# Performance work log

Hardware: AMD Instinct MI355X
Metric: run time of the kernel (lower is better)

Reference implementation:

```python
import jax, jax.numpy as jnp
import numpy as np

B, S, D, H = 2, 1536, 1024, 16
DK = D // H
NEG = -1e9
WEIGHT = 1.0  # undefined global `Weight` in source; treated as scalar 1.0


def setup_inputs() -> dict:
    key = jax.random.key(0)
    ks = jax.random.split(key, 16)
    inp = {
        "query": jax.random.normal(ks[0], (B, S, D), jnp.float32),
        "key": jax.random.normal(ks[1], (B, S, D), jnp.float32),
        "value": jax.random.normal(ks[2], (B, S, D), jnp.float32),
        "mask": jax.random.randint(ks[3], (B, 1, 1, S), 0, 2, jnp.int32),
        "mask1": jax.random.randint(ks[4], (B, 1, S, S), 0, 2, jnp.int32).astype(jnp.float32),
        "Wq": jax.random.normal(ks[5], (D, D), jnp.float32) / np.sqrt(D),
        "bq": jnp.zeros((D,), jnp.float32),
        "Wk": jax.random.normal(ks[6], (D, D), jnp.float32) / np.sqrt(D),
        "bk": jnp.zeros((D,), jnp.float32),
        "Wv": jax.random.normal(ks[7], (D, D), jnp.float32) / np.sqrt(D),
        "bv": jnp.zeros((D,), jnp.float32),
        "Wo": jax.random.normal(ks[8], (D, D), jnp.float32) / np.sqrt(D),
        "bo": jnp.zeros((D,), jnp.float32),
    }
    return inp


def _split_heads(x):
    # [B,S,D] -> [B,H,S,DK]
    return x.reshape(B, S, H, DK).transpose(0, 2, 1, 3)


def reference(query, key, value, mask, mask1, Wq, bq, Wk, bk, Wv, bv, Wo, bo):
    q = _split_heads(query @ Wq.T + bq)
    k = _split_heads(key @ Wk.T + bk)
    v = _split_heads(value @ Wv.T + bv)

    scores = jnp.einsum("bhqd,bhkd->bhqk", q, k) / jnp.sqrt(jnp.float32(DK))
    # softmax of mask1 over the query axis (dim=-2), zeros masked out
    m1 = jnp.where(mask1 == 0, NEG, mask1)
    m1s = jax.nn.softmax(m1, axis=-2)
    scores = (1.0 + m1s * mask1) * scores * WEIGHT
    scores = jnp.where(mask == 0, NEG, scores)
    p = jax.nn.softmax(scores, axis=-1)  # dropout: eval mode (identity)
    x = jnp.einsum("bhqk,bhkd->bhqd", p, v)
    x = x.transpose(0, 2, 1, 3).reshape(B, S, D)
    ret = x @ Wo.T + bo
    return ret, scores
```

## Files before the change

kernel.cpp:

```cpp
#include <hip/hip_runtime.h>
#include <hip/hip_bf16.h>

#define B_ 2
#define S_ 1536
#define D_ 1024
#define H_ 16
#define DK_ 64
#define KW_ 48
#define NT_ 24

#define RET_ELEMS 3145728

typedef __attribute__((ext_vector_type(8))) short short8;
typedef __attribute__((ext_vector_type(8))) unsigned short ushort8v;
typedef __attribute__((ext_vector_type(4))) unsigned short ushort4v;
typedef __attribute__((ext_vector_type(4))) float f32x4;

__device__ __forceinline__ unsigned short bf16_rne(float f) {
    return __builtin_bit_cast(unsigned short, __float2bfloat16(f));
}

struct CvtJobs {
    const float* src[7];
    unsigned short* dst[7];
    int n8[7];
};

__global__ __launch_bounds__(256) void cvt_kernel(CvtJobs j) {
    const int y = blockIdx.y;
    const int i = blockIdx.x * 256 + threadIdx.x;
    if (i >= j.n8[y]) return;
    const float* s = j.src[y] + (size_t)i * 8;
    float4 f0 = *(const float4*)s;
    float4 f1 = *(const float4*)(s + 4);
    ushort8v u;
    u[0]=bf16_rne(f0.x); u[1]=bf16_rne(f0.y); u[2]=bf16_rne(f0.z); u[3]=bf16_rne(f0.w);
    u[4]=bf16_rne(f1.x); u[5]=bf16_rne(f1.y); u[6]=bf16_rne(f1.z); u[7]=bf16_rne(f1.w);
    *(ushort8v*)(j.dst[y] + (size_t)i * 8) = u;
}

__global__ void bitpack_kernel(const float* __restrict__ mask1, unsigned int* __restrict__ bits,
                               float* __restrict__ colsum) {
    if (blockIdx.x < 12) colsum[blockIdx.x * 256 + threadIdx.x] = 0.f;
    const size_t gid = (size_t)blockIdx.x * 256 + threadIdx.x;
    const float v = mask1[gid];
    const unsigned long long bal = __ballot(v != 0.f);
    const int l = threadIdx.x & 63;
    if (l == 0)       bits[gid >> 5] = (unsigned int)bal;
    else if (l == 32) bits[gid >> 5] = (unsigned int)(bal >> 32);
}

__global__ void colcount_bits_kernel(const unsigned int* __restrict__ bits, float* __restrict__ colsum) {
    const int b     = blockIdx.x / 6;
    const int chunk = blockIdx.x % 6;
    const int col   = chunk * 256 + threadIdx.x;
    const int q0    = blockIdx.y * 96;
    const int wword = col >> 5, bit = col & 31;
    const unsigned int* p = bits + ((size_t)b * S_ + q0) * KW_ + wword;
    int s = 0;
    #pragma unroll 8
    for (int q = 0; q < 96; ++q) s += (p[(size_t)q * KW_] >> bit) & 1u;
    atomicAdd(&colsum[b * S_ + col], (float)s);
}

struct Proj { const unsigned short* A; const unsigned short* W; const float* bias; unsigned short* C; };

__global__ __launch_bounds__(512) void qkv_gemm_kernel(Proj p0, Proj p1, Proj p2) {
    const int bid = blockIdx.x;
    const int xcd = bid & 7, idx = bid >> 3;
    const int zy = xcd * 9 + (idx >> 3);
    const int bx = idx & 7;
    const int z = zy / 24, by = zy % 24;

    const unsigned short* A = z == 0 ? p0.A    : (z == 1 ? p1.A    : p2.A);
    const unsigned short* W = z == 0 ? p0.W    : (z == 1 ? p1.W    : p2.W);
    const float* bias       = z == 0 ? p0.bias : (z == 1 ? p1.bias : p2.bias);
    unsigned short* C       = z == 0 ? p0.C    : (z == 1 ? p1.C    : p2.C);

    __shared__ unsigned short As[128][72];
    __shared__ unsigned short Bs[128][72];
    const int tid = threadIdx.x;
    const int w = tid >> 6, lane = tid & 63;
    const int g = lane >> 4, c = lane & 15;
    const int wm = w >> 2, wn = w & 3;
    const int m0 = by * 128, n0 = bx * 128;
    const int trow = tid >> 2;
    const int tcol = (tid & 3) * 16;

    f32x4 acc[4][2];
    #pragma unroll
    for (int m = 0; m < 4; ++m)
        #pragma unroll
        for (int n = 0; n < 2; ++n)
            acc[m][n] = f32x4{0.f, 0.f, 0.f, 0.f};

    for (int k0 = 0; k0 < D_; k0 += 64) {
        {
            const unsigned short* ap = A + (size_t)(m0 + trow) * D_ + k0 + tcol;
            *(ushort8v*)&As[trow][tcol]     = *(const ushort8v*)ap;
            *(ushort8v*)&As[trow][tcol + 8] = *(const ushort8v*)(ap + 8);
            const unsigned short* wp = W + (size_t)(n0 + trow) * D_ + k0 + tcol;
            *(ushort8v*)&Bs[trow][tcol]     = *(const ushort8v*)wp;
            *(ushort8v*)&Bs[trow][tcol + 8] = *(const ushort8v*)(wp + 8);
        }
        __syncthreads();
        #pragma unroll
        for (int kk = 0; kk < 2; ++kk) {
            short8 a[4], bb[2];
            #pragma unroll
            for (int m = 0; m < 4; ++m) a[m]  = *(const short8*)&As[wm * 64 + m * 16 + c][kk * 32 + g * 8];
            #pragma unroll
            for (int n = 0; n < 2; ++n) bb[n] = *(const short8*)&Bs[wn * 32 + n * 16 + c][kk * 32 + g * 8];
            __builtin_amdgcn_s_setprio(1);
            #pragma unroll
            for (int m = 0; m < 4; ++m)
                #pragma unroll
                for (int n = 0; n < 2; ++n)
                    acc[m][n] = __builtin_amdgcn_mfma_f32_16x16x32_bf16(a[m], bb[n], acc[m][n], 0, 0, 0);
            __builtin_amdgcn_s_setprio(0);
        }
        __syncthreads();
    }
    #pragma unroll
    for (int n = 0; n < 2; ++n) {
        const int col = n0 + wn * 32 + n * 16 + c;
        const float bval = bias[col];
        #pragma unroll
        for (int m = 0; m < 4; ++m) {
            const int row0 = m0 + wm * 64 + m * 16 + g * 4;
            #pragma unroll
            for (int r = 0; r < 4; ++r)
                C[(size_t)(row0 + r) * D_ + col] = bf16_rne(acc[m][n][r] + bval);
        }
    }
}

__global__ __launch_bounds__(256) void out_gemm_kernel(
    const unsigned short* __restrict__ A, const unsigned short* __restrict__ W,
    const float* __restrict__ bias, float* __restrict__ C)
{
    const int bid = blockIdx.x;
    const int xcd = bid & 7, idx = bid >> 3;
    const int yg = xcd * 6 + (idx >> 4);
    const int bx = idx & 15;

    __shared__ unsigned short As[64][72];
    __shared__ unsigned short Bs[64][72];
    const int tid = threadIdx.x;
    const int w = tid >> 6, lane = tid & 63;
    const int g = lane >> 4, c = lane & 15;
    const int wm = w >> 1, wn = w & 1;
    const int m0 = yg * 64, n0 = bx * 64;
    const int trow = tid >> 2;
    const int tcol = (tid & 3) * 16;

    f32x4 acc[2][2];
    #pragma unroll
    for (int m = 0; m < 2; ++m)
        #pragma unroll
        for (int n = 0; n < 2; ++n)
            acc[m][n] = f32x4{0.f, 0.f, 0.f, 0.f};

    for (int k0 = 0; k0 < D_; k0 += 64) {
        {
            const unsigned short* ap = A + (size_t)(m0 + trow) * D_ + k0 + tcol;
            *(ushort8v*)&As[trow][tcol]     = *(const ushort8v*)ap;
            *(ushort8v*)&As[trow][tcol + 8] = *(const ushort8v*)(ap + 8);
            const unsigned short* wp = W + (size_t)(n0 + trow) * D_ + k0 + tcol;
            *(ushort8v*)&Bs[trow][tcol]     = *(const ushort8v*)wp;
            *(ushort8v*)&Bs[trow][tcol + 8] = *(const ushort8v*)(wp + 8);
        }
        __syncthreads();
        #pragma unroll
        for (int kk = 0; kk < 2; ++kk) {
            short8 a[2], bb[2];
            #pragma unroll
            for (int m = 0; m < 2; ++m) a[m]  = *(const short8*)&As[wm * 32 + m * 16 + c][kk * 32 + g * 8];
            #pragma unroll
            for (int n = 0; n < 2; ++n) bb[n] = *(const short8*)&Bs[wn * 32 + n * 16 + c][kk * 32 + g * 8];
            __builtin_amdgcn_s_setprio(1);
            #pragma unroll
            for (int m = 0; m < 2; ++m)
                #pragma unroll
                for (int n = 0; n < 2; ++n)
                    acc[m][n] = __builtin_amdgcn_mfma_f32_16x16x32_bf16(a[m], bb[n], acc[m][n], 0, 0, 0);
            __builtin_amdgcn_s_setprio(0);
        }
        __syncthreads();
    }
    #pragma unroll
    for (int n = 0; n < 2; ++n) {
        const int col = n0 + wn * 32 + n * 16 + c;
        const float bval = bias[col];
        #pragma unroll
        for (int m = 0; m < 2; ++m) {
            const int row0 = m0 + wm * 32 + m * 16 + g * 4;
            #pragma unroll
            for (int r = 0; r < 4; ++r)
                C[(size_t)(row0 + r) * D_ + col] = acc[m][n][r] + bval;
        }
    }
}

__global__ __launch_bounds__(512) void attn_kernel(
    const unsigned short* __restrict__ Qb, const unsigned short* __restrict__ Kb,
    const unsigned short* __restrict__ Vb, const int* __restrict__ mask,
    const unsigned int* __restrict__ bits, const float* __restrict__ colsum,
    float* __restrict__ scores, unsigned short* __restrict__ X)
{
    const int bid = blockIdx.x;
    const int xcd = bid & 7, idx = bid >> 3;
    const int grp = xcd * 4 + idx / 12;
    const int qt  = idx % 12;
    const int h = grp & 15, b = grp >> 4;

    const int tid = threadIdx.x;
    const int w = tid >> 6, lane = tid & 63;
    const int g = lane >> 4, c = lane & 15;

    __shared__ unsigned short VT_lds[2][64][72];
    __shared__ unsigned short P_lds[8][16][72];
    __shared__ float fac_lds[S_];

    for (int i = tid; i < S_; i += 512) {
        const int km = mask[b * S_ + i];
        const float cnt = colsum[b * S_ + i];
        fac_lds[i] = (km == 0) ? -1.f : ((cnt > 0.f) ? (1.f / cnt) : 0.f);
    }

    const int qrow0 = qt * 128 + w * 16;
    const unsigned short* qptr = Qb + ((size_t)b * S_ + qrow0 + c) * D_ + h * DK_;
    const short8 qf0 = *(const short8*)(qptr + g * 8);
    const short8 qf1 = *(const short8*)(qptr + 32 + g * 8);

    float mrow = -INFINITY, lrow = 0.f;
    f32x4 o[4];
    #pragma unroll
    for (int n = 0; n < 4; ++n) o[n] = f32x4{0.f, 0.f, 0.f, 0.f};

    float* srow = scores + ((((size_t)(b * H_ + h)) * S_ + qrow0 + c) * S_);
    const unsigned int* brow = bits + ((size_t)b * S_ + qrow0 + c) * KW_;
    const int kr = tid & 63, half = tid >> 6;
    const unsigned short* vrow = Vb + ((size_t)b * S_ + kr) * D_ + h * DK_ + half * 8;

    {
        short8 v0 = *(const short8*)vrow;
        #pragma unroll
        for (int j = 0; j < 8; ++j)
            VT_lds[0][half * 8 + j][kr] = (unsigned short)v0[j];
    }
    __syncthreads();

    for (int kt = 0; kt < NT_; ++kt) {
        const int k0 = kt * 64;
        const int cur = kt & 1;
        const bool have_next = (kt + 1) < NT_;

        short8 nv0;
        if (have_next) nv0 = *(const short8*)(vrow + (size_t)(k0 + 64) * D_);

        f32x4 sacc[4];
        #pragma unroll
        for (int n = 0; n < 4; ++n) sacc[n] = f32x4{0.f, 0.f, 0.f, 0.f};
        short8 kf0[4], kf1[4];
        #pragma unroll
        for (int n = 0; n < 4; ++n) {
            const unsigned short* kp = Kb + ((size_t)b * S_ + k0 + n * 16 + c) * D_ + h * DK_;
            kf0[n] = *(const short8*)(kp + g * 8);
            kf1[n] = *(const short8*)(kp + 32 + g * 8);
        }
        __builtin_amdgcn_s_setprio(1);
        #pragma unroll
        for (int n = 0; n < 4; ++n) {
            sacc[n] = __builtin_amdgcn_mfma_f32_16x16x32_bf16(kf0[n], qf0, sacc[n], 0, 0, 0);
            sacc[n] = __builtin_amdgcn_mfma_f32_16x16x32_bf16(kf1[n], qf1, sacc[n], 0, 0, 0);
        }
        __builtin_amdgcn_s_setprio(0);

        const unsigned int w0 = brow[(k0 >> 5)];
        const unsigned int w1 = brow[(k0 >> 5) + 1];
        float pmax = -INFINITY;
        f32x4 sv[4];
        #pragma unroll
        for (int n = 0; n < 4; ++n) {
            const f32x4 fv = *(const f32x4*)&fac_lds[k0 + n * 16 + g * 4];
            const unsigned int wsel = (n < 2) ? w0 : w1;
            #pragma unroll
            for (int r = 0; r < 4; ++r) {
                const int kl = n * 16 + g * 4 + r;
                const float f = fv[r];
                const float icnt = fmaxf(f, 0.f);
                const float bit = (float)((wsel >> (kl & 31)) & 1u);
                float s = sacc[n][r] * 0.125f * (1.f + bit * icnt);
                s = (f < 0.f) ? -1e9f : s;
                sv[n][r] = s;
                pmax = fmaxf(pmax, s);
            }
            __builtin_nontemporal_store(sv[n], (f32x4*)&srow[k0 + n * 16 + g * 4]);
        }

        pmax = fmaxf(pmax, __shfl_xor(pmax, 16));
        pmax = fmaxf(pmax, __shfl_xor(pmax, 32));
        const float nm = fmaxf(mrow, pmax);
        const float scq = __expf(mrow - nm);
        mrow = nm;
        lrow *= scq;
        float sc_o[4];
        #pragma unroll
        for (int r = 0; r < 4; ++r) sc_o[r] = __shfl(scq, (lane & 48) | (g * 4 + r));
        #pragma unroll
        for (int n = 0; n < 4; ++n)
            #pragma unroll
            for (int r = 0; r < 4; ++r) o[n][r] *= sc_o[r];

        #pragma unroll
        for (int n = 0; n < 4; ++n) {
            ushort4v pu;
            #pragma unroll
            for (int r = 0; r < 4; ++r) {
                const float p = __expf(sv[n][r] - mrow);
                lrow += p;
                pu[r] = bf16_rne(p);
            }
            *(ushort4v*)&P_lds[w][c][n * 16 + g * 4] = pu;
        }

        if (have_next) {
            #pragma unroll
            for (int j = 0; j < 8; ++j)
                VT_lds[cur ^ 1][half * 8 + j][kr] = (unsigned short)nv0[j];
        }

        __builtin_amdgcn_s_setprio(1);
        #pragma unroll
        for (int kk = 0; kk < 2; ++kk) {
            const short8 pa = *(const short8*)&P_lds[w][c][kk * 32 + g * 8];
            #pragma unroll
            for (int n = 0; n < 4; ++n) {
                const short8 vf = *(const short8*)&VT_lds[cur][n * 16 + c][kk * 32 + g * 8];
                o[n] = __builtin_amdgcn_mfma_f32_16x16x32_bf16(pa, vf, o[n], 0, 0, 0);
            }
        }
        __builtin_amdgcn_s_setprio(0);
        __syncthreads();
    }

    lrow += __shfl_xor(lrow, 16);
    lrow += __shfl_xor(lrow, 32);
    const float linv = 1.f / lrow;
    float linv_o[4];
    #pragma unroll
    for (int r = 0; r < 4; ++r) linv_o[r] = __shfl(linv, (lane & 48) | (g * 4 + r));
    #pragma unroll
    for (int n = 0; n < 4; ++n)
        #pragma unroll
        for (int r = 0; r < 4; ++r) {
            const size_t idx = ((size_t)b * S_ + qrow0 + g * 4 + r) * D_ + h * DK_ + n * 16 + c;
            X[idx] = bf16_rne(o[n][r] * linv_o[r]);
        }
}

extern "C" void kernel_launch(void* const* d_in, const int* in_sizes, int n_in,
                              void* d_out, int out_size, void* d_ws, size_t ws_size,
                              hipStream_t stream) {
    const float* query = (const float*)d_in[0];
    const float* key   = (const float*)d_in[1];
    const float* value = (const float*)d_in[2];
    const int*   mask  = (const int*)d_in[3];
    const float* mask1 = (const float*)d_in[4];
    const float* Wq = (const float*)d_in[5];
    const float* bq = (const float*)d_in[6];
    const float* Wk = (const float*)d_in[7];
    const float* bk = (const float*)d_in[8];
    const float* Wv = (const float*)d_in[9];
    const float* bv = (const float*)d_in[10];
    const float* Wo = (const float*)d_in[11];
    const float* bo = (const float*)d_in[12];

    float* ret_out    = (float*)d_out;
    float* scores_out = ret_out + RET_ELEMS;

    const size_t SZ = (size_t)B_ * S_ * D_;
    const size_t WZ = (size_t)D_ * D_;
    float* colsum = (float*)d_ws;
    unsigned int* bits = (unsigned int*)((char*)d_ws + 16384);
    unsigned short* Qb  = (unsigned short*)((char*)d_ws + 16384 + 589824);
    unsigned short* Kb  = Qb + SZ;
    unsigned short* Vb  = Kb + SZ;
    unsigned short* Xb  = Vb + SZ;
    unsigned short* qf  = Xb + SZ;
    unsigned short* kf  = qf + SZ;
    unsigned short* vf  = kf + SZ;
    unsigned short* Wqb = vf + SZ;
    unsigned short* Wkb = Wqb + WZ;
    unsigned short* Wvb = Wkb + WZ;
    unsigned short* Wob = Wvb + WZ;

    CvtJobs jobs;
    jobs.src[0] = query; jobs.dst[0] = qf;  jobs.n8[0] = (int)(SZ / 8);
    jobs.src[1] = key;   jobs.dst[1] = kf;  jobs.n8[1] = (int)(SZ / 8);
    jobs.src[2] = value; jobs.dst[2] = vf;  jobs.n8[2] = (int)(SZ / 8);
    jobs.src[3] = Wq;    jobs.dst[3] = Wqb; jobs.n8[3] = (int)(WZ / 8);
    jobs.src[4] = Wk;    jobs.dst[4] = Wkb; jobs.n8[4] = (int)(WZ / 8);
    jobs.src[5] = Wv;    jobs.dst[5] = Wvb; jobs.n8[5] = (int)(WZ / 8);
    jobs.src[6] = Wo;    jobs.dst[6] = Wob; jobs.n8[6] = (int)(WZ / 8);
    cvt_kernel<<<dim3((int)(SZ / 8 / 256), 7), 256, 0, stream>>>(jobs);

    bitpack_kernel<<<(B_ * S_ * S_) / 256, 256, 0, stream>>>(mask1, bits, colsum);
    colcount_bits_kernel<<<dim3(12, 16), 256, 0, stream>>>(bits, colsum);

    Proj p0{qf, Wqb, bq, Qb}, p1{kf, Wkb, bk, Kb}, p2{vf, Wvb, bv, Vb};
    qkv_gemm_kernel<<<576, 512, 0, stream>>>(p0, p1, p2);

    attn_kernel<<<384, 512, 0, stream>>>(Qb, Kb, Vb, mask, bits, colsum, scores_out, Xb);

    out_gemm_kernel<<<768, 256, 0, stream>>>(Xb, Wob, bo, ret_out);
}
```

Baseline: 232.3 us.

## Fuse bitpack with bf16 conversion and halve attention block query tile

Merges the mask bit-packing kernel and the fp32-to-bf16 conversion kernel into one launch whose flat grid carries no idle blocks for the smaller weight jobs. Separately, the attention kernel moves from 512-thread blocks covering 128 query rows to 256-thread blocks covering 64 rows, which doubles the grid to 768 blocks. Each thread now loads and transposes twice as much V per tile. The aim is to cut launch overhead and wasted blocks, and to improve occupancy and load balance in the attention kernel. The cost is that K/V tiles are re-read by twice as many blocks.

```diff
diff --git a/kernel.cpp b/kernel.cpp
--- a/kernel.cpp
+++ b/kernel.cpp
@@ -10,6 +10,7 @@
 #define NT_ 24
 
 #define RET_ELEMS 3145728
+#define BITPACK_BLOCKS 18432
 
 typedef __attribute__((ext_vector_type(8))) short short8;
 typedef __attribute__((ext_vector_type(8))) unsigned short ushort8v;
@@ -23,31 +24,35 @@
 struct CvtJobs {
     const float* src[7];
     unsigned short* dst[7];
-    int n8[7];
 };
 
-__global__ __launch_bounds__(256) void cvt_kernel(CvtJobs j) {
-    const int y = blockIdx.y;
-    const int i = blockIdx.x * 256 + threadIdx.x;
-    if (i >= j.n8[y]) return;
-    const float* s = j.src[y] + (size_t)i * 8;
+__global__ __launch_bounds__(256) void preproc_kernel(
+    const float* __restrict__ mask1, unsigned int* __restrict__ bits,
+    float* __restrict__ colsum, CvtJobs j)
+{
+    const int blk = blockIdx.x;
+    if (blk < BITPACK_BLOCKS) {
+        if (blk < 12) colsum[blk * 256 + threadIdx.x] = 0.f;
+        const size_t gid = (size_t)blk * 256 + threadIdx.x;
+        const float v = mask1[gid];
+        const unsigned long long bal = __ballot(v != 0.f);
+        const int l = threadIdx.x & 63;
+        if (l == 0)       bits[gid >> 5] = (unsigned int)bal;
+        else if (l == 32) bits[gid >> 5] = (unsigned int)(bal >> 32);
+        return;
+    }
+    int rb = blk - BITPACK_BLOCKS;
+    int job, base;
+    if (rb < 4608) { job = rb / 1536; base = rb % 1536; }
+    else { rb -= 4608; job = 3 + rb / 512; base = rb % 512; }
+    const size_t i = ((size_t)base * 256 + threadIdx.x) * 8;
+    const float* s = j.src[job] + i;
     float4 f0 = *(const float4*)s;
     float4 f1 = *(const float4*)(s + 4);
     ushort8v u;
     u[0]=bf16_rne(f0.x); u[1]=bf16_rne(f0.y); u[2]=bf16_rne(f0.z); u[3]=bf16_rne(f0.w);
     u[4]=bf16_rne(f1.x); u[5]=bf16_rne(f1.y); u[6]=bf16_rne(f1.z); u[7]=bf16_rne(f1.w);
-    *(ushort8v*)(j.dst[y] + (size_t)i * 8) = u;
-}
-
-__global__ void bitpack_kernel(const float* __restrict__ mask1, unsigned int* __restrict__ bits,
-                               float* __restrict__ colsum) {
-    if (blockIdx.x < 12) colsum[blockIdx.x * 256 + threadIdx.x] = 0.f;
-    const size_t gid = (size_t)blockIdx.x * 256 + threadIdx.x;
-    const float v = mask1[gid];
-    const unsigned long long bal = __ballot(v != 0.f);
-    const int l = threadIdx.x & 63;
-    if (l == 0)       bits[gid >> 5] = (unsigned int)bal;
-    else if (l == 32) bits[gid >> 5] = (unsigned int)(bal >> 32);
+    *(ushort8v*)(j.dst[job] + i) = u;
 }
 
 __global__ void colcount_bits_kernel(const unsigned int* __restrict__ bits, float* __restrict__ colsum) {
@@ -202,7 +207,7 @@
     }
 }
 
-__global__ __launch_bounds__(512) void attn_kernel(
+__global__ __launch_bounds__(256) void attn_kernel(
     const unsigned short* __restrict__ Qb, const unsigned short* __restrict__ Kb,
     const unsigned short* __restrict__ Vb, const int* __restrict__ mask,
     const unsigned int* __restrict__ bits, const float* __restrict__ colsum,
@@ -210,8 +215,8 @@
 {
     const int bid = blockIdx.x;
     const int xcd = bid & 7, idx = bid >> 3;
-    const int grp = xcd * 4 + idx / 12;
-    const int qt  = idx % 12;
+    const int grp = xcd * 4 + idx / 24;
+    const int qt  = idx % 24;
     const int h = grp & 15, b = grp >> 4;
 
     const int tid = threadIdx.x;
@@ -219,16 +224,16 @@
     const int g = lane >> 4, c = lane & 15;
 
     __shared__ unsigned short VT_lds[2][64][72];
-    __shared__ unsigned short P_lds[8][16][72];
+    __shared__ unsigned short P_lds[4][16][72];
     __shared__ float fac_lds[S_];
 
-    for (int i = tid; i < S_; i += 512) {
+    for (int i = tid; i < S_; i += 256) {
         const int km = mask[b * S_ + i];
         const float cnt = colsum[b * S_ + i];
         fac_lds[i] = (km == 0) ? -1.f : ((cnt > 0.f) ? (1.f / cnt) : 0.f);
     }
 
-    const int qrow0 = qt * 128 + w * 16;
+    const int qrow0 = qt * 64 + w * 16;
     const unsigned short* qptr = Qb + ((size_t)b * S_ + qrow0 + c) * D_ + h * DK_;
     const short8 qf0 = *(const short8*)(qptr + g * 8);
     const short8 qf1 = *(const short8*)(qptr + 32 + g * 8);
@@ -241,13 +246,16 @@
     float* srow = scores + ((((size_t)(b * H_ + h)) * S_ + qrow0 + c) * S_);
     const unsigned int* brow = bits + ((size_t)b * S_ + qrow0 + c) * KW_;
     const int kr = tid & 63, half = tid >> 6;
-    const unsigned short* vrow = Vb + ((size_t)b * S_ + kr) * D_ + h * DK_ + half * 8;
+    const unsigned short* vrow = Vb + ((size_t)b * S_ + kr) * D_ + h * DK_ + half * 16;
 
     {
         short8 v0 = *(const short8*)vrow;
-        #pragma unroll
-        for (int j = 0; j < 8; ++j)
-            VT_lds[0][half * 8 + j][kr] = (unsigned short)v0[j];
+        short8 v1 = *(const short8*)(vrow + 8);
+        #pragma unroll
+        for (int j = 0; j < 8; ++j) {
+            VT_lds[0][half * 16 + j][kr]     = (unsigned short)v0[j];
+            VT_lds[0][half * 16 + 8 + j][kr] = (unsigned short)v1[j];
+        }
     }
     __syncthreads();
 
@@ -256,8 +264,12 @@
         const int cur = kt & 1;
         const bool have_next = (kt + 1) < NT_;
 
-        short8 nv0;
-        if (have_next) nv0 = *(const short8*)(vrow + (size_t)(k0 + 64) * D_);
+        short8 nv0, nv1;
+        if (have_next) {
+            const unsigned short* vs = vrow + (size_t)(k0 + 64) * D_;
+            nv0 = *(const short8*)vs;
+            nv1 = *(const short8*)(vs + 8);
+        }
 
         f32x4 sacc[4];
         #pragma unroll
@@ -327,8 +339,10 @@
 
         if (have_next) {
             #pragma unroll
-            for (int j = 0; j < 8; ++j)
-                VT_lds[cur ^ 1][half * 8 + j][kr] = (unsigned short)nv0[j];
+            for (int j = 0; j < 8; ++j) {
+                VT_lds[cur ^ 1][half * 16 + j][kr]     = (unsigned short)nv0[j];
+                VT_lds[cur ^ 1][half * 16 + 8 + j][kr] = (unsigned short)nv1[j];
+            }
         }
 
         __builtin_amdgcn_s_setprio(1);
@@ -397,22 +411,21 @@
     unsigned short* Wob = Wvb + WZ;
 
     CvtJobs jobs;
-    jobs.src[0] = query; jobs.dst[0] = qf;  jobs.n8[0] = (int)(SZ / 8);
-    jobs.src[1] = key;   jobs.dst[1] = kf;  jobs.n8[1] = (int)(SZ / 8);
-    jobs.src[2] = value; jobs.dst[2] = vf;  jobs.n8[2] = (int)(SZ / 8);
-    jobs.src[3] = Wq;    jobs.dst[3] = Wqb; jobs.n8[3] = (int)(WZ / 8);
-    jobs.src[4] = Wk;    jobs.dst[4] = Wkb; jobs.n8[4] = (int)(WZ / 8);
-    jobs.src[5] = Wv;    jobs.dst[5] = Wvb; jobs.n8[5] = (int)(WZ / 8);
-    jobs.src[6] = Wo;    jobs.dst[6] = Wob; jobs.n8[6] = (int)(WZ / 8);
-    cvt_kernel<<<dim3((int)(SZ / 8 / 256), 7), 256, 0, stream>>>(jobs);
-
-    bitpack_kernel<<<(B_ * S_ * S_) / 256, 256, 0, stream>>>(mask1, bits, colsum);
+    jobs.src[0] = query; jobs.dst[0] = qf;
+    jobs.src[1] = key;   jobs.dst[1] = kf;
+    jobs.src[2] = value; jobs.dst[2] = vf;
+    jobs.src[3] = Wq;    jobs.dst[3] = Wqb;
+    jobs.src[4] = Wk;    jobs.dst[4] = Wkb;
+    jobs.src[5] = Wv;    jobs.dst[5] = Wvb;
+    jobs.src[6] = Wo;    jobs.dst[6] = Wob;
+
+    preproc_kernel<<<BITPACK_BLOCKS + 3 * 1536 + 4 * 512, 256, 0, stream>>>(mask1, bits, colsum, jobs);
     colcount_bits_kernel<<<dim3(12, 16), 256, 0, stream>>>(bits, colsum);
 
     Proj p0{qf, Wqb, bq, Qb}, p1{kf, Wkb, bk, Kb}, p2{vf, Wvb, bv, Vb};
     qkv_gemm_kernel<<<576, 512, 0, stream>>>(p0, p1, p2);
 
-    attn_kernel<<<384, 512, 0, stream>>>(Qb, Kb, Vb, mask, bits, colsum, scores_out, Xb);
+    attn_kernel<<<768, 256, 0, stream>>>(Qb, Kb, Vb, mask, bits, colsum, scores_out, Xb);
 
     out_gemm_kernel<<<768, 256, 0, stream>>>(Xb, Wob, bo, ret_out);
 }
```

Result: faster. 201.6 us (-13.2%).
